# Kernel tuning notes

Hardware: AMD Instinct MI355X
Metric: run time of the kernel (lower is better)

## Reference

```python
import itertools
import jax, jax.numpy as jnp
import numpy as np


def setup_inputs() -> dict:
    key = jax.random.key(0)
    k1, k2 = jax.random.split(key)
    B = 4
    F = (128, 128, 128)  # fixed image grid
    M = (128, 128, 128)  # moving image dims
    ddf = jax.random.normal(k1, (B, *F, 3), dtype=jnp.float32)
    image = jax.random.normal(k2, (B, *M), dtype=jnp.float32)
    return {"ddf": ddf, "image": image}


def _warp(image, ddf):
    # image: (B, m1, m2, m3); ddf: (B, f1, f2, f3, 3)
    B = image.shape[0]
    m_dims = image.shape[1:4]
    f_dims = ddf.shape[1:4]
    # reference grid in voxel coordinates of the fixed image
    grid = jnp.stack(
        jnp.meshgrid(*(jnp.arange(s, dtype=ddf.dtype) for s in f_dims), indexing="ij"),
        axis=-1,
    )  # (f1, f2, f3, 3)
    loc = grid[None] + ddf  # sample locations in moving-image voxel coords
    max_f = jnp.asarray([d - 1 for d in m_dims], dtype=ddf.dtype)
    loc = jnp.clip(loc, 0.0, max_f)  # boundary clamp (as in neurite resample)
    loc0 = jnp.floor(loc)
    w1 = loc - loc0  # trilinear weights toward the upper corner
    i0 = loc0.astype(jnp.int32)
    i1 = jnp.minimum(i0 + 1, jnp.asarray([d - 1 for d in m_dims], dtype=jnp.int32))
    bidx = jnp.arange(B)[:, None, None, None]
    out = jnp.zeros((B,) + f_dims, dtype=image.dtype)
    # 8-corner gather + weighted sum
    for corner in itertools.product((0, 1), repeat=3):
        idx = [(i1 if corner[a] else i0)[..., a] for a in range(3)]
        w = jnp.ones((), dtype=image.dtype)
        for a in range(3):
            w = w * (w1[..., a] if corner[a] else (1.0 - w1[..., a]))
        out = out + w * image[bidx, idx[0], idx[1], idx[2]]
    return out


def reference(ddf, image):
    return _warp(image, ddf)
```

## Files before the change

kernel.cpp:

```cpp
#include <hip/hip_runtime.h>


#define DIM 128
#define HALO 4
#define TX 8
#define TY 8
#define TZ 16
#define RX (TX + 2*HALO + 1)
#define RY (TY + 2*HALO + 1)
#define RZ (TZ + 2*HALO + 1)
#define RSZ (RX * RY * RZ)

typedef float vfloat4 __attribute__((ext_vector_type(4)));

__global__ __launch_bounds__(256) void warp_kernel(
    const float* __restrict__ ddf,
    const float* __restrict__ image,
    float* __restrict__ out)
{
    __shared__ float tile[RSZ];

    int bid = blockIdx.x;
    int zb = bid & 7;
    int yb = (bid >> 3) & 15;
    int xb = (bid >> 7) & 15;
    int b  = bid >> 11;

    int x0 = xb << 3, y0 = yb << 3, z0 = zb << 4;

    int rx0 = min(max(x0 - HALO, 0), DIM - RX);
    int ry0 = min(max(y0 - HALO, 0), DIM - RY);
    int rz0 = min(max(z0 - HALO, 0), DIM - RZ);

    int tid = threadIdx.x;

    int txy = tid >> 2;
    int x = x0 + (txy >> 3);
    int y = y0 + (txy & 7);
    int zbase = z0 + ((tid & 3) << 2);

    int v0 = (b << 21) + (x << 14) + (y << 7) + zbase;

    const vfloat4* dv = (const vfloat4*)(ddf + (size_t)v0 * 3);
    vfloat4 p0 = __builtin_nontemporal_load(dv + 0);
    vfloat4 p1 = __builtin_nontemporal_load(dv + 1);
    vfloat4 p2 = __builtin_nontemporal_load(dv + 2);

    const float* img = image + ((size_t)b << 21);

    for (int i = tid; i < RSZ; i += 256) {
        int rx  = i / (RY * RZ);
        int rem = i - rx * (RY * RZ);
        int ry  = rem / RZ;
        int rz  = rem - ry * RZ;
        tile[i] = img[((rx0 + rx) << 14) + ((ry0 + ry) << 7) + (rz0 + rz)];
    }
    __syncthreads();

    float dxl[4] = {p0.x, p0.w, p1.z, p2.y};
    float dyl[4] = {p0.y, p1.x, p1.w, p2.z};
    float dzl[4] = {p0.z, p1.y, p2.x, p2.w};

    const float maxf = (float)(DIM - 1);
    vfloat4 r;

#pragma unroll
    for (int j = 0; j < 4; ++j) {
        float lx = (float)x + dxl[j];
        float ly = (float)y + dyl[j];
        float lz = (float)(zbase + j) + dzl[j];
        lx = fminf(fmaxf(lx, 0.0f), maxf);
        ly = fminf(fmaxf(ly, 0.0f), maxf);
        lz = fminf(fmaxf(lz, 0.0f), maxf);
        float fx = floorf(lx), fy = floorf(ly), fz = floorf(lz);
        int ix0 = (int)fx, iy0 = (int)fy, iz0 = (int)fz;
        int ix1 = min(ix0 + 1, DIM - 1);
        int iy1 = min(iy0 + 1, DIM - 1);
        int iz1 = min(iz0 + 1, DIM - 1);
        float wx1 = lx - fx, wy1 = ly - fy, wz1 = lz - fz;

        bool inReg = (ix0 >= rx0) & (ix1 <= rx0 + RX - 1)
                   & (iy0 >= ry0) & (iy1 <= ry0 + RY - 1)
                   & (iz0 >= rz0) & (iz1 <= rz0 + RZ - 1);

        float c000, c001, c010, c011, c100, c101, c110, c111;
        if (inReg) {
            int la  = ((ix0 - rx0) * RY + (iy0 - ry0)) * RZ + (iz0 - rz0);
            int ddx = (ix1 - ix0) * (RY * RZ);
            int ddy = (iy1 - iy0) * RZ;
            int ddz = (iz1 - iz0);
            c000 = tile[la];             c001 = tile[la + ddz];
            c010 = tile[la + ddy];       c011 = tile[la + ddy + ddz];
            c100 = tile[la + ddx];       c101 = tile[la + ddx + ddz];
            c110 = tile[la + ddx + ddy]; c111 = tile[la + ddx + ddy + ddz];
        } else {
            int bx0 = ix0 << 14, bx1 = ix1 << 14;
            int by0 = iy0 << 7,  by1 = iy1 << 7;
            c000 = img[bx0 + by0 + iz0]; c001 = img[bx0 + by0 + iz1];
            c010 = img[bx0 + by1 + iz0]; c011 = img[bx0 + by1 + iz1];
            c100 = img[bx1 + by0 + iz0]; c101 = img[bx1 + by0 + iz1];
            c110 = img[bx1 + by1 + iz0]; c111 = img[bx1 + by1 + iz1];
        }

        float wz0w = 1.0f - wz1, wy0w = 1.0f - wy1, wx0w = 1.0f - wx1;
        float lo = wy0w * (wz0w * c000 + wz1 * c001) +
                   wy1  * (wz0w * c010 + wz1 * c011);
        float hi = wy0w * (wz0w * c100 + wz1 * c101) +
                   wy1  * (wz0w * c110 + wz1 * c111);
        r[j] = wx0w * lo + wx1 * hi;
    }

    __builtin_nontemporal_store(r, (vfloat4*)(out + v0));
}

extern "C" void kernel_launch(void* const* d_in, const int* in_sizes, int n_in,
                              void* d_out, int out_size, void* d_ws, size_t ws_size,
                              hipStream_t stream) {
    const float* ddf   = (const float*)d_in[0];
    const float* image = (const float*)d_in[1];
    float* out = (float*)d_out;

    int grid = 4 * 16 * 16 * 8;
    warp_kernel<<<grid, 256, 0, stream>>>(ddf, image, out);
}
```

Baseline: 217.1 us.

## Load halo tile via direct global-to-LDS 16-byte loads with padded z extent

Replaces the scalar per-element tile fill with unrolled __builtin_amdgcn_global_load_lds 16-byte transfers that write straight into shared memory, widening the z extent to 28 so each row is a multiple of four floats. The goal is to cut the VGPR round-trip and the per-element integer division overhead of staging the halo tile. It also rewrites the trilinear interpolation as a lerp chain of FMAs to reduce ALU work. The larger z halo raises LDS use to 32KB, which may limit occupancy. The 16-byte loads also read some padding elements past the region, with a clamp kept on the final offset.

```diff
diff --git a/kernel.cpp b/kernel.cpp
--- a/kernel.cpp
+++ b/kernel.cpp
@@ -3,13 +3,11 @@
 
 #define DIM 128
 #define HALO 4
-#define TX 8
-#define TY 8
-#define TZ 16
-#define RX (TX + 2*HALO + 1)
-#define RY (TY + 2*HALO + 1)
-#define RZ (TZ + 2*HALO + 1)
-#define RSZ (RX * RY * RZ)
+#define RX 17
+#define RY 17
+#define ZP 28
+#define PLANE (RY * ZP)
+#define RSZ 8192
 
 typedef float vfloat4 __attribute__((ext_vector_type(4)));
 
@@ -30,7 +28,7 @@
 
     int rx0 = min(max(x0 - HALO, 0), DIM - RX);
     int ry0 = min(max(y0 - HALO, 0), DIM - RY);
-    int rz0 = min(max(z0 - HALO, 0), DIM - RZ);
+    int rz0 = min(max(z0 - HALO, 0), DIM - ZP);
 
     int tid = threadIdx.x;
 
@@ -38,7 +36,6 @@
     int x = x0 + (txy >> 3);
     int y = y0 + (txy & 7);
     int zbase = z0 + ((tid & 3) << 2);
-
     int v0 = (b << 21) + (x << 14) + (y << 7) + zbase;
 
     const vfloat4* dv = (const vfloat4*)(ddf + (size_t)v0 * 3);
@@ -48,12 +45,23 @@
 
     const float* img = image + ((size_t)b << 21);
 
-    for (int i = tid; i < RSZ; i += 256) {
-        int rx  = i / (RY * RZ);
-        int rem = i - rx * (RY * RZ);
-        int ry  = rem / RZ;
-        int rz  = rem - ry * RZ;
-        tile[i] = img[((rx0 + rx) << 14) + ((ry0 + ry) << 7) + (rz0 + rz)];
+    {
+        int base0 = (rx0 << 14) + (ry0 << 7) + rz0;
+        int t4 = tid << 2;
+#pragma unroll
+        for (int k = 0; k < 8; ++k) {
+            int i = (k << 10) + t4;
+            int rx  = i / PLANE;
+            int rem = i - rx * PLANE;
+            int ry  = rem / ZP;
+            int rz  = rem - ry * ZP;
+            int goff = base0 + (rx << 14) + (ry << 7) + rz;
+            goff = min(goff, (1 << 21) - 4);
+            __builtin_amdgcn_global_load_lds(
+                (const __attribute__((address_space(1))) void*)(img + goff),
+                (__attribute__((address_space(3))) void*)(tile + i),
+                16, 0, 0);
+        }
     }
     __syncthreads();
 
@@ -81,13 +89,13 @@
 
         bool inReg = (ix0 >= rx0) & (ix1 <= rx0 + RX - 1)
                    & (iy0 >= ry0) & (iy1 <= ry0 + RY - 1)
-                   & (iz0 >= rz0) & (iz1 <= rz0 + RZ - 1);
+                   & (iz0 >= rz0) & (iz1 <= rz0 + ZP - 1);
 
         float c000, c001, c010, c011, c100, c101, c110, c111;
         if (inReg) {
-            int la  = ((ix0 - rx0) * RY + (iy0 - ry0)) * RZ + (iz0 - rz0);
-            int ddx = (ix1 - ix0) * (RY * RZ);
-            int ddy = (iy1 - iy0) * RZ;
+            int la  = (ix0 - rx0) * PLANE + (iy0 - ry0) * ZP + (iz0 - rz0);
+            int ddx = (ix1 - ix0) * PLANE;
+            int ddy = (iy1 - iy0) * ZP;
             int ddz = (iz1 - iz0);
             c000 = tile[la];             c001 = tile[la + ddz];
             c010 = tile[la + ddy];       c011 = tile[la + ddy + ddz];
@@ -102,12 +110,13 @@
             c110 = img[bx1 + by1 + iz0]; c111 = img[bx1 + by1 + iz1];
         }
 
-        float wz0w = 1.0f - wz1, wy0w = 1.0f - wy1, wx0w = 1.0f - wx1;
-        float lo = wy0w * (wz0w * c000 + wz1 * c001) +
-                   wy1  * (wz0w * c010 + wz1 * c011);
-        float hi = wy0w * (wz0w * c100 + wz1 * c101) +
-                   wy1  * (wz0w * c110 + wz1 * c111);
-        r[j] = wx0w * lo + wx1 * hi;
+        float c00 = __builtin_fmaf(wz1, c001 - c000, c000);
+        float c01 = __builtin_fmaf(wz1, c011 - c010, c010);
+        float c10 = __builtin_fmaf(wz1, c101 - c100, c100);
+        float c11 = __builtin_fmaf(wz1, c111 - c110, c110);
+        float c0  = __builtin_fmaf(wy1, c01 - c00, c00);
+        float c1  = __builtin_fmaf(wy1, c11 - c10, c10);
+        r[j]      = __builtin_fmaf(wx1, c1 - c0, c0);
     }
 
     __builtin_nontemporal_store(r, (vfloat4*)(out + v0));
```

Result: faster. 206.7 us (-4.8%).
